# Optimization experiments

Hardware: AMD Instinct MI355X
Metric: run time of the kernel (lower is better)

## Reference

```python
import jax, jax.numpy as jnp
import numpy as np

N_NODES = 16384
K_NBR = 16
N_HOPS = 4  # hops + 2
IN_DIM = 256
RAW_DIM = 128
OUT_DIM = 64
PHI_DIM = 16
N_KERN = 4
E = N_NODES * K_NBR


def setup_inputs() -> dict:
    key = jax.random.key(0)
    ks = jax.random.split(key, 16)
    s = 0.05  # small weight scale for numerical sanity
    h = jax.random.normal(ks[0], (N_NODES, IN_DIM), jnp.float32)
    e_tensor = jax.random.normal(ks[1], (N_HOPS, N_NODES, RAW_DIM), jnp.float32)
    # kNN-style edges: each dst node has exactly K_NBR incoming edges
    src = jax.random.randint(ks[2], (N_HOPS, E), 0, N_NODES, jnp.int32)
    dst = jnp.tile(jnp.repeat(jnp.arange(N_NODES, dtype=jnp.int32), K_NBR)[None, :], (N_HOPS, 1))
    return {
        'h': h,
        'e_tensor': e_tensor,
        'src': src,
        'dst': dst,
        'W_phi': jax.random.normal(ks[3], (N_HOPS, RAW_DIM, PHI_DIM - 1), jnp.float32) * s,
        'mlp_w1': jax.random.normal(ks[4], (N_HOPS, RAW_DIM, IN_DIM), jnp.float32) * s,
        'mlp_b1': jax.random.normal(ks[5], (N_HOPS, IN_DIM), jnp.float32) * s,
        'mlp_w2': jax.random.normal(ks[6], (N_HOPS, IN_DIM, PHI_DIM * N_KERN), jnp.float32) * s,
        'mlp_b2': jax.random.normal(ks[7], (N_HOPS, PHI_DIM * N_KERN), jnp.float32) * s,
        'tilde_phi': jax.random.normal(ks[8], (N_HOPS, N_KERN, PHI_DIM), jnp.float32),
        'W': jax.random.normal(ks[9], (N_HOPS, IN_DIM, OUT_DIM * N_KERN), jnp.float32) * s,
        'bias': jax.random.normal(ks[10], (N_HOPS, OUT_DIM), jnp.float32) * s,
        'z': jax.random.normal(ks[11], (OUT_DIM, 1), jnp.float32),
    }


def _deform_gconv(h, e_l, src, dst, W_phi, w1, b1, w2, b2, tilde_phi, W, bias):
    N = h.shape[0]
    nk, phi_dim = tilde_phi.shape
    hk = (h @ W).reshape(N, nk, -1)                                  # (N, nk, out)
    phi = e_l @ W_phi                                                # (N, phi-1)
    tn = tilde_phi / jnp.linalg.norm(tilde_phi, axis=1, keepdims=True)  # (nk, phi)
    hid = jax.nn.relu(e_l @ w1 + b1)
    delta = (hid @ w2 + b2).reshape(N, nk, phi_dim)                  # (N, nk, phi)
    delta_ik = tn[None, :, :] + delta                                # (N, nk, phi)
    # per-edge quantities (edges carry dst-node delta_ik, u_sub_v distance)
    dist = phi[src] - phi[dst]                                       # (E, phi-1)
    last = jnp.all(dist == 0, axis=1, keepdims=True).astype(dist.dtype)
    dist = jnp.concatenate([dist, last], axis=1)                     # (E, phi)
    dist = dist / jnp.maximum(jnp.linalg.norm(dist, axis=1, keepdims=True), 1e-8)
    logits = jnp.einsum('ep,ekp->ek', dist, delta_ik[dst])           # (E, nk)
    # edge_softmax over incoming edges of each dst node
    mx = jax.ops.segment_max(logits, dst, num_segments=N)
    ex = jnp.exp(logits - mx[dst])
    den = jax.ops.segment_sum(ex, dst, num_segments=N)
    att = ex / den[dst]                                              # (E, nk)
    # message passing: m = h[src] * att, sum over incoming edges
    m = hk[src] * att[:, :, None]                                    # (E, nk, out)
    agg = jax.ops.segment_sum(m, dst, num_segments=N)                # (N, nk, out)
    out = agg.sum(1) + bias[None, :]
    out = out / jnp.maximum(jnp.linalg.norm(out, axis=1, keepdims=True), 1e-8)
    # regularizers
    d = tn[:, None, :] - tn[None, :, :]                              # (nk, nk, phi)
    l_sep = jnp.sum(jnp.sum(d * d, axis=-1)) / nk                    # sum_i mean_j ||t_i - t_j||^2
    l_focus = jnp.mean(jnp.sum(delta * delta, axis=2))
    return out, l_sep, l_focus


def reference(h, e_tensor, src, dst, W_phi, mlp_w1, mlp_b1, mlp_w2, mlp_b2, tilde_phi, W, bias, z):
    outs, l_seps, l_fos = jax.vmap(
        _deform_gconv, in_axes=(None, 0, 0, 0, 0, 0, 0, 0, 0, 0, 0, 0)
    )(h, e_tensor, src, dst, W_phi, mlp_w1, mlp_b1, mlp_w2, mlp_b2, tilde_phi, W, bias)
    # hop-level softmax fusion
    score = jnp.einsum('hno,oz->hnz', outs, z)                       # (n_hops, N, 1)
    att = jax.nn.softmax(score, axis=0)
    tilde_h = jnp.sum(att * outs, axis=0)                            # (N, out)
    l_sep = jnp.mean(l_seps)
    l_focus = jnp.mean(l_fos)
    return tilde_h, l_sep, l_focus
```

## Files before the change

### kernel.cpp

```cpp
#include <hip/hip_runtime.h>
#include <hip/hip_bf16.h>

#define N_NODES 16384
#define K_NBR 16
#define HOPS 4
#define IN_DIM 256
#define RAW_DIM 128
#define OUT_DIM 64
#define PHI_DIM 16
#define N_KERN 4
#define E_EDGES (N_NODES * K_NBR)

typedef __hip_bfloat16 bf16;
typedef __attribute__((ext_vector_type(8))) short short8;
typedef __attribute__((ext_vector_type(4))) float f32x4;
typedef __attribute__((ext_vector_type(4))) unsigned int uint4v;

__device__ __forceinline__ float toF(float x) { return x; }
__device__ __forceinline__ float toF(bf16 x) { return __bfloat162float(x); }
__device__ __forceinline__ short f2bfbits(float f)
{
    bf16 b = __float2bfloat16(f);
    short s; __builtin_memcpy(&s, &b, 2); return s;
}

#define CV_WPHI 0
#define CV_W1   (CV_WPHI + HOPS * RAW_DIM * (PHI_DIM - 1))
#define CV_B1   (CV_W1 + HOPS * RAW_DIM * IN_DIM)
#define CV_W2   (CV_B1 + HOPS * IN_DIM)
#define CV_B2   (CV_W2 + HOPS * IN_DIM * PHI_DIM * N_KERN)
#define CV_TPHI (CV_B2 + HOPS * PHI_DIM * N_KERN)
#define CV_W    (CV_TPHI + HOPS * N_KERN * PHI_DIM)
#define CV_BIAS (CV_W + HOPS * IN_DIM * OUT_DIM * N_KERN)
#define CV_Z    (CV_BIAS + HOPS * OUT_DIM)
#define CV_END  (CV_Z + OUT_DIM)

#define WT_N  (HOPS * 256 * 256)
#define W1T_N (HOPS * 256 * 128)
#define W2T_N (HOPS * 64 * 256)
#define WPT_N (HOPS * 16 * 128)
#define CVT_TOTAL (WT_N + W1T_N + W2T_N + WPT_N)

#define NB_CV ((CV_END + 255) / 256)
#define NB_WT (CVT_TOTAL / 256)
#define NB_H  (N_NODES * 256 / 8 / 256)
#define NB_E  (HOPS * N_NODES * 128 / 8 / 256)
#define NB_ALL (NB_CV + NB_WT + NB_H + NB_E + 1)

__device__ __forceinline__ float loadDyn(const void* p, int i, bool isbf)
{
    return isbf ? toF(((const bf16*)p)[i]) : ((const float*)p)[i];
}

__device__ __forceinline__ void cvt8(bf16* dst, const void* src, size_t base, bool isbf)
{
    short8 v;
    if (isbf) {
        v = *(const short8*)((const bf16*)src + base);
    } else {
        const float* sp = (const float*)src + base;
        f32x4 f0 = *(const f32x4*)sp;
        f32x4 f1 = *(const f32x4*)(sp + 4);
#pragma unroll
        for (int j = 0; j < 4; j++) { v[j] = f2bfbits(f0[j]); v[4 + j] = f2bfbits(f1[j]); }
    }
    *(short8*)(dst + base) = v;
}

__global__ __launch_bounds__(256) void cvt_all(
    const void* h, const void* e,
    const void* wphi, const void* w1, const void* b1, const void* w2,
    const void* b2, const void* tphi, const void* W, const void* bias,
    const void* z, float* __restrict__ CV,
    bf16* __restrict__ wt, bf16* __restrict__ w1t, bf16* __restrict__ w2t,
    bf16* __restrict__ wpt, bf16* __restrict__ h_bf, bf16* __restrict__ e_bf,
    float* __restrict__ tn_out, float* __restrict__ acc, int* __restrict__ flagOut)
{
    __shared__ float s_det[4];
    int tid = threadIdx.x;
    {
        unsigned short pv = ((const unsigned short*)h)[tid];
        unsigned int bits = ((unsigned int)pv) << 16;
        float v; __builtin_memcpy(&v, &bits, 4);
        v = fabsf(v);
        if (!(v == v) || v > 1e30f) v = 1e30f;
#pragma unroll
        for (int off = 32; off > 0; off >>= 1) v = fmaxf(v, __shfl_xor(v, off));
        if ((tid & 63) == 0) s_det[tid >> 6] = v;
    }
    __syncthreads();
    bool isbf = fmaxf(fmaxf(s_det[0], s_det[1]), fmaxf(s_det[2], s_det[3])) < 1e4f;

    int b = blockIdx.x;
    if (b == NB_ALL - 1) {
        __shared__ float s_v[256], s_tn[256], s_red[256], s_hop[4];
        int hop = tid >> 6, t64 = tid & 63;
        int row = t64 >> 4, p = t64 & 15;
        float v = loadDyn(tphi, hop * 64 + t64, isbf);
        s_v[tid] = v;
        __syncthreads();
        float ss = 0.f;
        for (int q = 0; q < 16; q++) { float x = s_v[hop * 64 + row * 16 + q]; ss += x * x; }
        float tnv = v / sqrtf(ss);
        tn_out[hop * 64 + t64] = tnv;
        s_tn[tid] = tnv;
        __syncthreads();
        float s = 0.f;
        for (int j = 0; j < 4; j++) {
            float d = tnv - s_tn[hop * 64 + j * 16 + p];
            s += d * d;
        }
        s_red[tid] = s;
        __syncthreads();
        if (t64 == 0) {
            float tot = 0.f;
            for (int i = 0; i < 64; i++) tot += s_red[hop * 64 + i];
            s_hop[hop] = tot;
        }
        __syncthreads();
        if (tid == 0) {
            acc[0] = (s_hop[0] + s_hop[1] + s_hop[2] + s_hop[3]) * 0.0625f;
            acc[1] = 0.f;
            *flagOut = isbf ? 1 : 0;
        }
        return;
    }
    if (b < NB_CV) {
        int idx = b * 256 + tid;
        if (idx >= CV_END) return;
        float v;
        if      (idx < CV_W1)   v = loadDyn(wphi, idx - CV_WPHI, isbf);
        else if (idx < CV_B1)   v = loadDyn(w1,   idx - CV_W1,   isbf);
        else if (idx < CV_W2)   v = loadDyn(b1,   idx - CV_B1,   isbf);
        else if (idx < CV_B2)   v = loadDyn(w2,   idx - CV_W2,   isbf);
        else if (idx < CV_TPHI) v = loadDyn(b2,   idx - CV_B2,   isbf);
        else if (idx < CV_W)    v = loadDyn(tphi, idx - CV_TPHI, isbf);
        else if (idx < CV_BIAS) v = loadDyn(W,    idx - CV_W,    isbf);
        else if (idx < CV_Z)    v = loadDyn(bias, idx - CV_BIAS, isbf);
        else                    v = loadDyn(z,    idx - CV_Z,    isbf);
        CV[idx] = v;
        return;
    }
    b -= NB_CV;
    if (b < NB_WT) {
        int idx = b * 256 + tid;
        if (idx < WT_N) {
            int o = idx, hop = o >> 16, rem = o & 65535, n = rem >> 8, k = rem & 255;
            wt[o] = __float2bfloat16(loadDyn(W, hop * 65536 + k * 256 + n, isbf));
        } else if (idx < WT_N + W1T_N) {
            int o = idx - WT_N, hop = o >> 15, rem = o & 32767, n = rem >> 7, k = rem & 127;
            w1t[o] = __float2bfloat16(loadDyn(w1, hop * 32768 + k * 256 + n, isbf));
        } else if (idx < WT_N + W1T_N + W2T_N) {
            int o = idx - WT_N - W1T_N, hop = o >> 14, rem = o & 16383, n = rem >> 8, k = rem & 255;
            w2t[o] = __float2bfloat16(loadDyn(w2, hop * 16384 + k * 64 + n, isbf));
        } else {
            int o = idx - WT_N - W1T_N - W2T_N, hop = o >> 11, rem = o & 2047, n = rem >> 7, k = rem & 127;
            float v = (n < 15) ? loadDyn(wphi, hop * 1920 + k * 15 + n, isbf) : 0.f;
            wpt[o] = __float2bfloat16(v);
        }
        return;
    }
    b -= NB_WT;
    if (b < NB_H) {
        size_t base = ((size_t)b * 256 + tid) * 8;
        cvt8(h_bf, h, base, isbf);
        return;
    }
    b -= NB_H;
    {
        size_t base = ((size_t)b * 256 + tid) * 8;
        cvt8(e_bf, e, base, isbf);
    }
}

template <int BN, int WR, int WC, int OUTMODE, bool STAGED>
__device__ __forceinline__ void gemm_dev(
    char* smem, const bf16* __restrict__ A, const bf16* __restrict__ Bt,
    void* __restrict__ Cg, int K, int N, int colBase)
{
    constexpr int WM = 128 / WR;
    constexpr int WN = BN / WC;
    constexpr int MT = WM / 16;
    constexpr int NT = WN / 16;
    constexpr int ESZ = (OUTMODE == 0) ? 4 : 1;
    short* As = (short*)smem;
    short* Bs = As + 128 * 72;

    int tid = threadIdx.x;
    int w = tid >> 6, lane = tid & 63;
    int wr = w / WC, wc = w % WC;
    int l16 = lane & 15, quad = lane >> 4;
    int rowBase = blockIdx.y * 128;

    f32x4 acc[MT][NT] = {};

    for (int k0 = 0; k0 < K; k0 += 64) {
        for (int c = tid; c < 128 * 8; c += 256) {
            int row = c >> 3, c8 = c & 7;
            *(short8*)&As[row * 72 + c8 * 8] =
                *(const short8*)(A + (size_t)(rowBase + row) * K + k0 + c8 * 8);
        }
        for (int c = tid; c < BN * 8; c += 256) {
            int row = c >> 3, c8 = c & 7;
            *(short8*)&Bs[row * 72 + c8 * 8] =
                *(const short8*)(Bt + (size_t)(colBase + row) * K + k0 + c8 * 8);
        }
        __syncthreads();
#pragma unroll
        for (int kc = 0; kc < 64; kc += 32) {
            short8 aF[MT], bF[NT];
#pragma unroll
            for (int mi = 0; mi < MT; mi++)
                aF[mi] = *(const short8*)&As[(wr * WM + mi * 16 + l16) * 72 + kc + quad * 8];
#pragma unroll
            for (int ni = 0; ni < NT; ni++)
                bF[ni] = *(const short8*)&Bs[(wc * WN + ni * 16 + l16) * 72 + kc + quad * 8];
#pragma unroll
            for (int mi = 0; mi < MT; mi++)
#pragma unroll
                for (int ni = 0; ni < NT; ni++)
                    acc[mi][ni] = __builtin_amdgcn_mfma_f32_16x16x32_bf16(
                        aF[mi], bF[ni], acc[mi][ni], 0, 0, 0);
        }
        __syncthreads();
    }

#pragma unroll
    for (int mi = 0; mi < MT; mi++) {
#pragma unroll
        for (int ni = 0; ni < NT; ni++) {
            int cl = wc * WN + ni * 16 + l16;
            int col = colBase + cl;
#pragma unroll
            for (int r = 0; r < 4; r++) {
                int rl = wr * WM + mi * 16 + quad * 4 + r;
                float v = acc[mi][ni][r];
                if (STAGED) {
                    size_t idx = (size_t)rl * BN + cl;
                    if (OUTMODE == 0) ((float*)smem)[idx] = v;
                    else {
                        int pk = __builtin_amdgcn_cvt_pk_fp8_f32(v, v, 0, false);
                        ((unsigned char*)smem)[idx] = (unsigned char)(pk & 0xFF);
                    }
                } else {
                    ((float*)Cg)[(size_t)(rowBase + rl) * N + col] = v;
                }
            }
        }
    }
    if (STAGED) {
        __syncthreads();
        constexpr int CPR = BN * ESZ / 16;
        for (int c = tid; c < 128 * CPR; c += 256) {
            int r = c / CPR, off = (c % CPR) * 16;
            *(uint4v*)((char*)Cg + ((size_t)(rowBase + r) * N + colBase) * ESZ + off) =
                *(const uint4v*)(smem + (size_t)r * BN * ESZ + off);
        }
    }
}

__global__ __launch_bounds__(256) void hkphi_kernel(
    const bf16* __restrict__ h_bf, const bf16* __restrict__ e_bf,
    const bf16* __restrict__ WT, const bf16* __restrict__ WPT,
    unsigned char* __restrict__ hk_f8, float* __restrict__ phi)
{
    __shared__ __align__(16) char smem[128 * 72 * 2 + 128 * 72 * 2];
    int hop = blockIdx.z;
    if (blockIdx.x < 2) {
        gemm_dev<128, 2, 2, 2, true>(
            smem, h_bf, WT + (size_t)hop * 256 * 256,
            hk_f8 + (size_t)hop * N_NODES * 256, 256, 256, blockIdx.x * 128);
    } else {
        gemm_dev<16, 4, 1, 0, false>(
            smem, e_bf + (size_t)hop * N_NODES * 128, WPT + (size_t)hop * 16 * 128,
            phi + (size_t)hop * N_NODES * 16, 128, 16, 0);
    }
}

__global__ __launch_bounds__(256) void hid_delta_kernel(
    const bf16* __restrict__ e_bf, const bf16* __restrict__ W1T,
    const bf16* __restrict__ W2T, const float* __restrict__ b1All,
    const float* __restrict__ b2All, const float* __restrict__ tnAll,
    float* __restrict__ DELTA, float* __restrict__ lfocus)
{
    __shared__ __align__(16) char smem[128 * 72 * 2 + 256 * 72 * 2 + 128 * 264 * 2];
    __shared__ float s_w[4];
    short* As = (short*)smem;
    short* Bs = As + 128 * 72;
    short* Hs = Bs + 256 * 72;
    float* Ds = (float*)smem;

    int hop = blockIdx.y;
    int rowBase = blockIdx.x * 128;
    const bf16* A  = e_bf + (size_t)hop * N_NODES * 128;
    const bf16* B1 = W1T + (size_t)hop * 256 * 128;
    const bf16* B2 = W2T + (size_t)hop * 64 * 256;
    const float* b1 = b1All + hop * 256;
    const float* b2 = b2All + hop * 64;
    const float* tn = tnAll + hop * 64;

    int tid = threadIdx.x;
    int w = tid >> 6, lane = tid & 63;
    int l16 = lane & 15, quad = lane >> 4;

    {
        int wr = w >> 1, wc = w & 1;
        f32x4 acc[4][8] = {};
        for (int k0 = 0; k0 < 128; k0 += 64) {
            for (int c = tid; c < 128 * 8; c += 256) {
                int row = c >> 3, c8 = c & 7;
                *(short8*)&As[row * 72 + c8 * 8] =
                    *(const short8*)(A + (size_t)(rowBase + row) * 128 + k0 + c8 * 8);
            }
            for (int c = tid; c < 256 * 8; c += 256) {
                int row = c >> 3, c8 = c & 7;
                *(short8*)&Bs[row * 72 + c8 * 8] =
                    *(const short8*)(B1 + (size_t)row * 128 + k0 + c8 * 8);
            }
            __syncthreads();
#pragma unroll
            for (int kc = 0; kc < 64; kc += 32) {
                short8 aF[4], bF[8];
#pragma unroll
                for (int mi = 0; mi < 4; mi++)
                    aF[mi] = *(const short8*)&As[(wr * 64 + mi * 16 + l16) * 72 + kc + quad * 8];
#pragma unroll
                for (int ni = 0; ni < 8; ni++)
                    bF[ni] = *(const short8*)&Bs[(wc * 128 + ni * 16 + l16) * 72 + kc + quad * 8];
#pragma unroll
                for (int mi = 0; mi < 4; mi++)
#pragma unroll
                    for (int ni = 0; ni < 8; ni++)
                        acc[mi][ni] = __builtin_amdgcn_mfma_f32_16x16x32_bf16(
                            aF[mi], bF[ni], acc[mi][ni], 0, 0, 0);
            }
            __syncthreads();
        }
#pragma unroll
        for (int mi = 0; mi < 4; mi++) {
#pragma unroll
            for (int ni = 0; ni < 8; ni++) {
                int col = wc * 128 + ni * 16 + l16;
                float bv = b1[col];
#pragma unroll
                for (int r = 0; r < 4; r++) {
                    int row = wr * 64 + mi * 16 + quad * 4 + r;
                    float v = fmaxf(acc[mi][ni][r] + bv, 0.f);
                    Hs[row * 264 + col] = f2bfbits(v);
                }
            }
        }
        __syncthreads();
    }

    {
        f32x4 acc[2][4] = {};
        for (int kc = 0; kc < 256; kc += 32) {
            short8 aF[2], bF[4];
#pragma unroll
            for (int mi = 0; mi < 2; mi++)
                aF[mi] = *(const short8*)&Hs[(w * 32 + mi * 16 + l16) * 264 + kc + quad * 8];
#pragma unroll
            for (int ni = 0; ni < 4; ni++)
                bF[ni] = *(const short8*)(B2 + (size_t)(ni * 16 + l16) * 256 + kc + quad * 8);
#pragma unroll
            for (int mi = 0; mi < 2; mi++)
#pragma unroll
                for (int ni = 0; ni < 4; ni++)
                    acc[mi][ni] = __builtin_amdgcn_mfma_f32_16x16x32_bf16(
                        aF[mi], bF[ni], acc[mi][ni], 0, 0, 0);
        }
        float sq = 0.f;
#pragma unroll
        for (int mi = 0; mi < 2; mi++) {
#pragma unroll
            for (int ni = 0; ni < 4; ni++) {
                int col = ni * 16 + l16;
                float bv = b2[col], tv = tn[col];
#pragma unroll
                for (int r = 0; r < 4; r++) {
                    int row = w * 32 + mi * 16 + quad * 4 + r;
                    float v = acc[mi][ni][r] + bv;
                    sq += v * v;
                    Ds[row * 64 + col] = v + tv;
                }
            }
        }
#pragma unroll
        for (int off = 32; off > 0; off >>= 1) sq += __shfl_xor(sq, off);
        if (lane == 0) s_w[w] = sq;
        __syncthreads();
        float* Dg = DELTA + (size_t)hop * N_NODES * 64;
        for (int c = tid; c < 128 * 16; c += 256) {
            int r = c >> 4, off = (c & 15) * 4;
            *(uint4v*)(Dg + (size_t)(rowBase + r) * 64 + off) =
                *(const uint4v*)(Ds + (size_t)r * 64 + off);
        }
        if (tid == 0) atomicAdd(lfocus, s_w[0] + s_w[1] + s_w[2] + s_w[3]);
    }
}

__global__ __launch_bounds__(256) void edge_agg2(
    const unsigned char* __restrict__ hk, const float* __restrict__ phi,
    const float* __restrict__ dik, const int* __restrict__ src,
    const float* __restrict__ biasAll, float* __restrict__ outs)
{
    int b = blockIdx.x;
    int hop = b & 3;
    int wave = threadIdx.x >> 6, lane = threadIdx.x & 63;
    int node = (b >> 2) * 4 + wave;
    const unsigned char* hk_l = hk + (size_t)hop * N_NODES * 256;
    const float* phi_l  = phi + (size_t)hop * N_NODES * 16;
    const float* dik_l  = dik + (size_t)hop * N_NODES * 64;
    const int*   src_n  = src + (size_t)hop * E_EDGES + (size_t)node * 16;
    const float* bias_l = biasAll + hop * 64;
    float*       outs_n = outs + ((size_t)hop * N_NODES + node) * 64;

    __shared__ float s_dik[4][64];
    __shared__ float s_attT[4][4][20];
    __shared__ int   s_src[4][16];

    s_dik[wave][lane] = dik_l[(size_t)node * 64 + lane];
    if (lane < 16) s_src[wave][lane] = src_n[lane];

    int e = lane >> 2, q = lane & 3;
    int sN = s_src[wave][e];
    f32x4 ps = *(const f32x4*)(phi_l + (size_t)sN * 16 + q * 4);
    f32x4 pd = *(const f32x4*)(phi_l + (size_t)node * 16 + q * 4);
    float d0 = ps[0] - pd[0], d1 = ps[1] - pd[1];
    float d2 = ps[2] - pd[2], d3 = ps[3] - pd[3];
    bool q3 = (q == 3);
    float nzf = ((d0 != 0.f) | (d1 != 0.f) | (d2 != 0.f) | (!q3 && d3 != 0.f)) ? 1.f : 0.f;
    float ssp = d0 * d0 + d1 * d1 + d2 * d2 + (q3 ? 0.f : d3 * d3);
    nzf += __shfl_xor(nzf, 1); nzf += __shfl_xor(nzf, 2);
    ssp += __shfl_xor(ssp, 1); ssp += __shfl_xor(ssp, 2);
    float last = (nzf == 0.f) ? 1.f : 0.f;
    if (q3) d3 = last;
    float inv = 1.f / fmaxf(sqrtf(ssp + last * last), 1e-8f);
#pragma unroll
    for (int k = 0; k < 4; k++) {
        const float* dk = &s_dik[wave][k * 16 + q * 4];
        float pk = d0 * dk[0] + d1 * dk[1] + d2 * dk[2] + d3 * dk[3];
        pk += __shfl_xor(pk, 1); pk += __shfl_xor(pk, 2);
        if (q == k) s_attT[wave][k][e] = pk * inv;
    }

    int k2 = lane & 3;
    float lgv = s_attT[wave][k2][e];
    float mx = lgv;
    mx = fmaxf(mx, __shfl_xor(mx, 4));
    mx = fmaxf(mx, __shfl_xor(mx, 8));
    mx = fmaxf(mx, __shfl_xor(mx, 16));
    mx = fmaxf(mx, __shfl_xor(mx, 32));
    float ex = expf(lgv - mx);
    float den = ex;
    den += __shfl_xor(den, 4);
    den += __shfl_xor(den, 8);
    den += __shfl_xor(den, 16);
    den += __shfl_xor(den, 32);
    s_attT[wave][k2][e] = ex / den;

    int kk = lane >> 4, dsub = (lane & 15) * 4;
    f32x4 attv[4];
#pragma unroll
    for (int g = 0; g < 4; g++) attv[g] = *(const f32x4*)&s_attT[wave][kk][g * 4];
    float a0 = 0.f, a1 = 0.f, a2 = 0.f, a3 = 0.f;
#pragma unroll
    for (int ee = 0; ee < 16; ee++) {
        int sm = __builtin_amdgcn_readfirstlane(s_src[wave][ee]);
        unsigned int u = *(const unsigned int*)(hk_l + (size_t)sm * 256 + lane * 4);
        float wgt = attv[ee >> 2][ee & 3];
        auto lo = __builtin_amdgcn_cvt_pk_f32_fp8((int)u, false);
        auto hi = __builtin_amdgcn_cvt_pk_f32_fp8((int)u, true);
        a0 += wgt * lo[0];
        a1 += wgt * lo[1];
        a2 += wgt * hi[0];
        a3 += wgt * hi[1];
    }
    a0 += __shfl_xor(a0, 16); a0 += __shfl_xor(a0, 32);
    a1 += __shfl_xor(a1, 16); a1 += __shfl_xor(a1, 32);
    a2 += __shfl_xor(a2, 16); a2 += __shfl_xor(a2, 32);
    a3 += __shfl_xor(a3, 16); a3 += __shfl_xor(a3, 32);
    float o0 = a0 + bias_l[dsub + 0];
    float o1 = a1 + bias_l[dsub + 1];
    float o2 = a2 + bias_l[dsub + 2];
    float o3 = a3 + bias_l[dsub + 3];
    float ssq = o0 * o0 + o1 * o1 + o2 * o2 + o3 * o3;
    ssq += __shfl_xor(ssq, 1);
    ssq += __shfl_xor(ssq, 2);
    ssq += __shfl_xor(ssq, 4);
    ssq += __shfl_xor(ssq, 8);
    float inv2 = 1.f / fmaxf(sqrtf(ssq), 1e-8f);
    if (kk == 0) {
        f32x4 st;
        st[0] = o0 * inv2; st[1] = o1 * inv2; st[2] = o2 * inv2; st[3] = o3 * inv2;
        *(f32x4*)(outs_n + dsub) = st;
    }
}

__global__ __launch_bounds__(256) void fuse_kernel(
    const float* __restrict__ outs, const float* __restrict__ z,
    void* __restrict__ out, const int* __restrict__ flag,
    const float* __restrict__ acc)
{
    int tid = threadIdx.x;
    int node = blockIdx.x * 4 + (tid >> 6);
    int dd = tid & 63;
    float zv = z[dd];
    float o[4], sc[4];
#pragma unroll
    for (int h = 0; h < 4; h++) {
        o[h] = outs[((size_t)h * N_NODES + node) * 64 + dd];
        float v = o[h] * zv;
#pragma unroll
        for (int off = 32; off > 0; off >>= 1) v += __shfl_xor(v, off);
        sc[h] = v;
    }
    float mx = fmaxf(fmaxf(sc[0], sc[1]), fmaxf(sc[2], sc[3]));
    float e0 = expf(sc[0] - mx), e1 = expf(sc[1] - mx);
    float e2 = expf(sc[2] - mx), e3 = expf(sc[3] - mx);
    float den = e0 + e1 + e2 + e3;
    float t = (e0 * o[0] + e1 * o[1] + e2 * o[2] + e3 * o[3]) / den;
    size_t oi = (size_t)node * 64 + dd;
    bool isbf = (*flag != 0);
    if (isbf) ((bf16*)out)[oi] = __float2bfloat16(t);
    else      ((float*)out)[oi] = t;
    if (blockIdx.x == 0 && tid == 0) {
        float a = acc[0];
        float b = acc[1] / ((float)N_NODES * 4.f * 4.f);
        size_t base = (size_t)N_NODES * 64;
        if (isbf) {
            ((bf16*)out)[base]     = __float2bfloat16(a);
            ((bf16*)out)[base + 1] = __float2bfloat16(b);
        } else {
            ((float*)out)[base]     = a;
            ((float*)out)[base + 1] = b;
        }
    }
}

extern "C" void kernel_launch(void* const* d_in, const int* in_sizes, int n_in,
                              void* d_out, int out_size, void* d_ws, size_t ws_size,
                              hipStream_t stream)
{
    const void* h    = d_in[0];
    const void* e    = d_in[1];
    const int*  src  = (const int*)d_in[2];
    const void* Wphi = d_in[4];
    const void* w1   = d_in[5];
    const void* b1   = d_in[6];
    const void* w2   = d_in[7];
    const void* b2   = d_in[8];
    const void* tphi = d_in[9];
    const void* W    = d_in[10];
    const void* bias = d_in[11];
    const void* z    = d_in[12];

    float* ws    = (float*)d_ws;
    float* CV    = ws;
    float* OUTS  = CV + CV_END;
    float* PHI   = OUTS + (size_t)4 * N_NODES * 64;
    float* DELTA = PHI + (size_t)4 * N_NODES * 16;
    float* TN    = DELTA + (size_t)4 * N_NODES * 64;
    float* ACC   = TN + 256;
    int*   FLAG  = (int*)(ACC + 2);
    bf16*  H_BF  = (bf16*)(ACC + 4);
    bf16*  E_BF  = H_BF + (size_t)N_NODES * 256;
    bf16*  WT    = E_BF + (size_t)HOPS * N_NODES * 128;
    bf16*  W1T   = WT + WT_N;
    bf16*  W2T   = W1T + W1T_N;
    bf16*  WPT   = W2T + W2T_N;
    unsigned char* HK_F8 = (unsigned char*)(WPT + WPT_N);

    cvt_all<<<NB_ALL, 256, 0, stream>>>(
        h, e, Wphi, w1, b1, w2, b2, tphi, W, bias, z, CV,
        WT, W1T, W2T, WPT, H_BF, E_BF, TN, ACC, FLAG);

    hkphi_kernel<<<dim3(3, 128, HOPS), 256, 0, stream>>>(
        H_BF, E_BF, WT, WPT, HK_F8, PHI);
    hid_delta_kernel<<<dim3(128, HOPS), 256, 0, stream>>>(
        E_BF, W1T, W2T, CV + CV_B1, CV + CV_B2, TN, DELTA, ACC + 1);
    edge_agg2<<<dim3(N_NODES), 256, 0, stream>>>(
        HK_F8, PHI, DELTA, src, CV + CV_BIAS, OUTS);

    fuse_kernel<<<dim3(N_NODES / 4), 256, 0, stream>>>(
        OUTS, CV + CV_Z, d_out, FLAG, ACC);
}
```

Baseline: 232.9 us.

## Halve hid_delta row tile, stage W2 in LDS, use fast exp

The hid/delta MLP kernel now processes 64 rows per block instead of 128, which doubles the grid to 1024 blocks and cuts per-wave accumulators and LDS use. The second-layer weight W2 is staged into shared memory, reusing the freed first-layer B buffer, instead of being read from global memory on every k-step. The edge and fuse softmaxes switch from expf to __expf, and the attention LDS array is padded and aligned. The smaller tile means W1 is loaded twice as often across blocks, and __expf gives up a little accuracy.

```diff
diff --git a/kernel.cpp b/kernel.cpp
--- a/kernel.cpp
+++ b/kernel.cpp
@@ -283,15 +283,16 @@
     const float* __restrict__ b2All, const float* __restrict__ tnAll,
     float* __restrict__ DELTA, float* __restrict__ lfocus)
 {
-    __shared__ __align__(16) char smem[128 * 72 * 2 + 256 * 72 * 2 + 128 * 264 * 2];
+    __shared__ __align__(16) char smem[64 * 72 * 2 + 256 * 72 * 2 + 64 * 264 * 2];
     __shared__ float s_w[4];
-    short* As = (short*)smem;
-    short* Bs = As + 128 * 72;
-    short* Hs = Bs + 256 * 72;
-    float* Ds = (float*)smem;
+    short* As  = (short*)smem;
+    short* Bs  = As + 64 * 72;
+    short* Hs  = Bs + 256 * 72;
+    short* B2s = Bs;
+    float* Ds  = (float*)smem;
 
     int hop = blockIdx.y;
-    int rowBase = blockIdx.x * 128;
+    int rowBase = blockIdx.x * 64;
     const bf16* A  = e_bf + (size_t)hop * N_NODES * 128;
     const bf16* B1 = W1T + (size_t)hop * 256 * 128;
     const bf16* B2 = W2T + (size_t)hop * 64 * 256;
@@ -304,10 +305,9 @@
     int l16 = lane & 15, quad = lane >> 4;
 
     {
-        int wr = w >> 1, wc = w & 1;
-        f32x4 acc[4][8] = {};
+        f32x4 acc[4][4] = {};
         for (int k0 = 0; k0 < 128; k0 += 64) {
-            for (int c = tid; c < 128 * 8; c += 256) {
+            for (int c = tid; c < 64 * 8; c += 256) {
                 int row = c >> 3, c8 = c & 7;
                 *(short8*)&As[row * 72 + c8 * 8] =
                     *(const short8*)(A + (size_t)(rowBase + row) * 128 + k0 + c8 * 8);
@@ -320,17 +320,17 @@
             __syncthreads();
 #pragma unroll
             for (int kc = 0; kc < 64; kc += 32) {
-                short8 aF[4], bF[8];
+                short8 aF[4], bF[4];
 #pragma unroll
                 for (int mi = 0; mi < 4; mi++)
-                    aF[mi] = *(const short8*)&As[(wr * 64 + mi * 16 + l16) * 72 + kc + quad * 8];
-#pragma unroll
-                for (int ni = 0; ni < 8; ni++)
-                    bF[ni] = *(const short8*)&Bs[(wc * 128 + ni * 16 + l16) * 72 + kc + quad * 8];
+                    aF[mi] = *(const short8*)&As[(mi * 16 + l16) * 72 + kc + quad * 8];
+#pragma unroll
+                for (int ni = 0; ni < 4; ni++)
+                    bF[ni] = *(const short8*)&Bs[(w * 64 + ni * 16 + l16) * 72 + kc + quad * 8];
 #pragma unroll
                 for (int mi = 0; mi < 4; mi++)
 #pragma unroll
-                    for (int ni = 0; ni < 8; ni++)
+                    for (int ni = 0; ni < 4; ni++)
                         acc[mi][ni] = __builtin_amdgcn_mfma_f32_16x16x32_bf16(
                             aF[mi], bF[ni], acc[mi][ni], 0, 0, 0);
             }
@@ -339,51 +339,49 @@
 #pragma unroll
         for (int mi = 0; mi < 4; mi++) {
 #pragma unroll
-            for (int ni = 0; ni < 8; ni++) {
-                int col = wc * 128 + ni * 16 + l16;
+            for (int ni = 0; ni < 4; ni++) {
+                int col = w * 64 + ni * 16 + l16;
                 float bv = b1[col];
 #pragma unroll
                 for (int r = 0; r < 4; r++) {
-                    int row = wr * 64 + mi * 16 + quad * 4 + r;
+                    int row = mi * 16 + quad * 4 + r;
                     float v = fmaxf(acc[mi][ni][r] + bv, 0.f);
                     Hs[row * 264 + col] = f2bfbits(v);
                 }
             }
         }
+        for (int c = tid; c < 64 * 32; c += 256) {
+            int row = c >> 5, ch = c & 31;
+            *(short8*)&B2s[row * 264 + ch * 8] =
+                *(const short8*)(B2 + (size_t)row * 256 + ch * 8);
+        }
         __syncthreads();
     }
 
     {
-        f32x4 acc[2][4] = {};
+        f32x4 acc2[4] = {};
         for (int kc = 0; kc < 256; kc += 32) {
-            short8 aF[2], bF[4];
-#pragma unroll
-            for (int mi = 0; mi < 2; mi++)
-                aF[mi] = *(const short8*)&Hs[(w * 32 + mi * 16 + l16) * 264 + kc + quad * 8];
+            short8 aF = *(const short8*)&Hs[(w * 16 + l16) * 264 + kc + quad * 8];
+            short8 bF[4];
 #pragma unroll
             for (int ni = 0; ni < 4; ni++)
-                bF[ni] = *(const short8*)(B2 + (size_t)(ni * 16 + l16) * 256 + kc + quad * 8);
-#pragma unroll
-            for (int mi = 0; mi < 2; mi++)
-#pragma unroll
-                for (int ni = 0; ni < 4; ni++)
-                    acc[mi][ni] = __builtin_amdgcn_mfma_f32_16x16x32_bf16(
-                        aF[mi], bF[ni], acc[mi][ni], 0, 0, 0);
-        }
+                bF[ni] = *(const short8*)&B2s[(ni * 16 + l16) * 264 + kc + quad * 8];
+#pragma unroll
+            for (int ni = 0; ni < 4; ni++)
+                acc2[ni] = __builtin_amdgcn_mfma_f32_16x16x32_bf16(aF, bF[ni], acc2[ni], 0, 0, 0);
+        }
+        __syncthreads();
         float sq = 0.f;
 #pragma unroll
-        for (int mi = 0; mi < 2; mi++) {
-#pragma unroll
-            for (int ni = 0; ni < 4; ni++) {
-                int col = ni * 16 + l16;
-                float bv = b2[col], tv = tn[col];
-#pragma unroll
-                for (int r = 0; r < 4; r++) {
-                    int row = w * 32 + mi * 16 + quad * 4 + r;
-                    float v = acc[mi][ni][r] + bv;
-                    sq += v * v;
-                    Ds[row * 64 + col] = v + tv;
-                }
+        for (int ni = 0; ni < 4; ni++) {
+            int col = ni * 16 + l16;
+            float bv = b2[col], tv = tn[col];
+#pragma unroll
+            for (int r = 0; r < 4; r++) {
+                int row = w * 16 + quad * 4 + r;
+                float v = acc2[ni][r] + bv;
+                sq += v * v;
+                Ds[row * 64 + col] = v + tv;
             }
         }
 #pragma unroll
@@ -391,7 +389,7 @@
         if (lane == 0) s_w[w] = sq;
         __syncthreads();
         float* Dg = DELTA + (size_t)hop * N_NODES * 64;
-        for (int c = tid; c < 128 * 16; c += 256) {
+        for (int c = tid; c < 64 * 16; c += 256) {
             int r = c >> 4, off = (c & 15) * 4;
             *(uint4v*)(Dg + (size_t)(rowBase + r) * 64 + off) =
                 *(const uint4v*)(Ds + (size_t)r * 64 + off);
@@ -417,7 +415,7 @@
     float*       outs_n = outs + ((size_t)hop * N_NODES + node) * 64;
 
     __shared__ float s_dik[4][64];
-    __shared__ float s_attT[4][4][20];
+    __shared__ __align__(16) float s_attT[4][4][24];
     __shared__ int   s_src[4][16];
 
     s_dik[wave][lane] = dik_l[(size_t)node * 64 + lane];
@@ -452,7 +450,7 @@
     mx = fmaxf(mx, __shfl_xor(mx, 8));
     mx = fmaxf(mx, __shfl_xor(mx, 16));
     mx = fmaxf(mx, __shfl_xor(mx, 32));
-    float ex = expf(lgv - mx);
+    float ex = __expf(lgv - mx);
     float den = ex;
     den += __shfl_xor(den, 4);
     den += __shfl_xor(den, 8);
@@ -517,8 +515,8 @@
         sc[h] = v;
     }
     float mx = fmaxf(fmaxf(sc[0], sc[1]), fmaxf(sc[2], sc[3]));
-    float e0 = expf(sc[0] - mx), e1 = expf(sc[1] - mx);
-    float e2 = expf(sc[2] - mx), e3 = expf(sc[3] - mx);
+    float e0 = __expf(sc[0] - mx), e1 = __expf(sc[1] - mx);
+    float e2 = __expf(sc[2] - mx), e3 = __expf(sc[3] - mx);
     float den = e0 + e1 + e2 + e3;
     float t = (e0 * o[0] + e1 * o[1] + e2 * o[2] + e3 * o[3]) / den;
     size_t oi = (size_t)node * 64 + dd;
@@ -578,7 +576,7 @@
 
     hkphi_kernel<<<dim3(3, 128, HOPS), 256, 0, stream>>>(
         H_BF, E_BF, WT, WPT, HK_F8, PHI);
-    hid_delta_kernel<<<dim3(128, HOPS), 256, 0, stream>>>(
+    hid_delta_kernel<<<dim3(N_NODES / 64, HOPS), 256, 0, stream>>>(
         E_BF, W1T, W2T, CV + CV_B1, CV + CV_B2, TN, DELTA, ACC + 1);
     edge_agg2<<<dim3(N_NODES), 256, 0, stream>>>(
         HK_F8, PHI, DELTA, src, CV + CV_BIAS, OUTS);
```

Measured after the change: 232.6 us. About the same (-0.1%).
